# Kernel optimization log

Measured on AMD Instinct MI355X. Metric: run time of the kernel, lower is better.

The kernel has to match this reference:

```python
import jax, jax.numpy as jnp
import numpy as np

# Config mirrors Voxelization(__init__) with training=True -> max_voxels[0]
VOXEL_SIZE = (0.05, 0.05, 0.1)
PC_LO = (0.0, -40.0, -3.0)
PC_HI = (70.4, 40.0, 1.0)
MAX_POINTS = 64
MAX_VOXELS = 60000
GX = int(round((PC_HI[0] - PC_LO[0]) / VOXEL_SIZE[0]))  # 1408
GY = int(round((PC_HI[1] - PC_LO[1]) / VOXEL_SIZE[1]))  # 1600
GZ = int(round((PC_HI[2] - PC_LO[2]) / VOXEL_SIZE[2]))  # 40
SENT = GX * GY * GZ  # sentinel linear id for out-of-range points


def setup_inputs() -> dict:
    key = jax.random.key(0)
    u = jax.random.uniform(key, (2_000_000, 4), dtype=jnp.float32)
    lo = jnp.array([PC_LO[0], PC_LO[1], PC_LO[2], 0.0], jnp.float32)
    span = jnp.array([PC_HI[0] - PC_LO[0], PC_HI[1] - PC_LO[1], PC_HI[2] - PC_LO[2], 1.0], jnp.float32)
    points = lo + u * span  # xyz inside range, intensity in [0,1)
    return {"points": points}


def _voxelize(points):
    N, C = points.shape
    vs = jnp.array(VOXEL_SIZE, jnp.float32)
    lo = jnp.array(PC_LO, jnp.float32)
    grid = jnp.array([GX, GY, GZ], jnp.int32)

    g = jnp.floor((points[:, :3] - lo) / vs).astype(jnp.int32)  # [N,3] grid coords (x,y,z)
    valid = jnp.all((g >= 0) & (g < grid), axis=1)
    lin = (g[:, 0] * GY + g[:, 1]) * GZ + g[:, 2]
    lin = jnp.where(valid, lin, SENT).astype(jnp.int32)

    # Stable sort by voxel id; ties keep original point order (deterministic mode)
    order = jnp.argsort(lin)  # jnp.argsort is stable
    sl = lin[order]
    idx = jnp.arange(N, dtype=jnp.int32)
    is_start = jnp.concatenate([jnp.ones((1,), bool), sl[1:] != sl[:-1]])
    gid_sorted = (jnp.cumsum(is_start) - 1).astype(jnp.int32)  # sorted-group id per sorted point

    # First original point index per group -> first-occurrence voxel ordering
    group_first = jnp.full((N,), N, jnp.int32).at[gid_sorted].min(
        jnp.where(is_start, order.astype(jnp.int32), N))
    group_lin = jnp.full((N,), SENT, jnp.int32).at[gid_sorted].min(sl)
    group_first = jnp.where(group_lin == SENT, N, group_first)  # sentinel group ranks last
    perm = jnp.argsort(group_first)  # rank -> group
    inv_rank = jnp.zeros((N,), jnp.int32).at[perm].set(idx)  # group -> rank

    num_valid = jnp.sum(is_start & (sl != SENT)).astype(jnp.int32)
    voxel_num = jnp.minimum(num_valid, MAX_VOXELS)

    # Position within voxel (point order within group)
    start_idx = jax.lax.cummax(jnp.where(is_start, idx, -1))
    pos_sorted = idx - start_idx

    gid = jnp.zeros((N,), jnp.int32).at[order].set(gid_sorted)
    pos = jnp.zeros((N,), jnp.int32).at[order].set(pos_sorted)
    rank = inv_rank[gid]
    keep = valid & (rank < MAX_VOXELS) & (pos < MAX_POINTS)
    rk = jnp.where(keep, rank, MAX_VOXELS)  # OOB -> dropped
    pk = jnp.where(keep, pos, MAX_POINTS)

    voxels = jnp.zeros((MAX_VOXELS, MAX_POINTS, C), points.dtype).at[rk, pk].set(points, mode='drop')
    coors = jnp.zeros((MAX_VOXELS, 3), jnp.int32).at[rk].set(g[:, ::-1], mode='drop')  # flip -> (z,y,x)
    group_count = jnp.zeros((N,), jnp.int32).at[gid_sorted].add((sl != SENT).astype(jnp.int32))
    npv = jnp.minimum(group_count[perm], MAX_POINTS)[:MAX_VOXELS].astype(jnp.int32)
    return voxels, coors, npv, voxel_num


def reference(points):
    # Padded equivalent of torch output (voxels[:n], coors[:n].flip(-1), npv[:n]):
    # rows >= voxel_num are zero; voxel_num gives the true count.
    return _voxelize(points)
```

## Files before the change

### kernel.cpp

```cpp
#include <hip/hip_runtime.h>


#define MAXV 60000
#define MAXP 64
#define FCUT 131072
#define NBUCK 512
#define BSHIFT 13
#define BSLOTS 8192
#define TMASK (NBUCK * BSLOTS - 1)
#define BCAP 5120
#define ECAP 512
#define BIN_CHUNK 4096
#define BIN_T 512
#define SCAN_T 1024
#define CHUNK 2048

typedef unsigned long long u64;

__device__ __forceinline__ int compute_lin(float x, float y, float z) {
  float fx = floorf((x - 0.0f) / 0.05f);
  float fy = floorf((y - (-40.0f)) / 0.05f);
  float fz = floorf((z - (-3.0f)) / 0.1f);
  if (!(fx >= 0.0f && fx < 1408.0f &&
        fy >= 0.0f && fy < 1600.0f &&
        fz >= 0.0f && fz < 40.0f))
    return -1;
  return (((int)fx) * 1600 + (int)fy) * 40 + (int)fz;
}

__device__ __forceinline__ unsigned hash_s(int lin) {
  unsigned h = (unsigned)lin * 2654435761u;
  return (h ^ (h >> 15)) & TMASK;
}

__global__ __launch_bounds__(BIN_T) void k_binA(const float4* __restrict__ pts,
                                                int N, u64* __restrict__ binned,
                                                int* __restrict__ bucketCnt) {
  __shared__ int hist[NBUCK];
  __shared__ int lbase[NBUCK];
  __shared__ int cursor[NBUCK];
  __shared__ int gbase[NBUCK];
  __shared__ int totSh;
  __shared__ u64 stage[BIN_CHUNK];

  int tid = threadIdx.x;
  int blockStart = blockIdx.x * BIN_CHUNK;
  hist[tid] = 0;
  __syncthreads();

  unsigned sArr[8];
  int linArr[8];
#pragma unroll
  for (int j = 0; j < 8; j++) {
    int i = blockStart + j * BIN_T + tid;
    unsigned sv = 0xFFFFFFFFu; int lv = 0;
    if (i < N) {
      float4 p = pts[i];
      int lin = compute_lin(p.x, p.y, p.z);
      if (lin >= 0) {
        sv = hash_s(lin);
        lv = lin;
        atomicAdd(&hist[sv >> BSHIFT], 1);
      }
    }
    sArr[j] = sv; linArr[j] = lv;
  }
  __syncthreads();

  int v = hist[tid];
  lbase[tid] = v;
  __syncthreads();
  for (int off = 1; off < NBUCK; off <<= 1) {
    int t = (tid >= off) ? lbase[tid - off] : 0;
    __syncthreads();
    lbase[tid] += t;
    __syncthreads();
  }
  int excl = lbase[tid] - v;
  __syncthreads();
  lbase[tid] = excl;
  cursor[tid] = excl;
  __syncthreads();

#pragma unroll
  for (int j = 0; j < 8; j++) {
    if (sArr[j] != 0xFFFFFFFFu) {
      int b = (int)(sArr[j] >> BSHIFT);
      int k = atomicAdd(&cursor[b], 1);
      int i = blockStart + j * BIN_T + tid;
      stage[k] = ((u64)(unsigned)linArr[j] << 32) | (unsigned)i;
    }
  }
  __syncthreads();

  int cntB = cursor[tid] - lbase[tid];
  if (cntB > 0) gbase[tid] = atomicAdd(&bucketCnt[tid], cntB);
  if (tid == BIN_T - 1) totSh = cursor[NBUCK - 1];
  __syncthreads();

  int tot = totSh;
  for (int k = tid; k < tot; k += BIN_T) {
    u64 e = stage[k];
    int b = (int)(hash_s((int)(e >> 32)) >> BSHIFT);
    int off = gbase[b] + (k - lbase[b]);
    if (off < BCAP) binned[(size_t)b * BCAP + off] = e;
  }
}

__global__ __launch_bounds__(1024) void k_binB(
    const u64* __restrict__ binned, const int* __restrict__ bucketCnt,
    u64* __restrict__ fs, u64* __restrict__ gEbuf, int* __restrict__ bcnt,
    int* __restrict__ occPartials) {
  __shared__ u64 tab[BSLOTS];
  __shared__ u64 ev[ECAP];
  __shared__ int evCnt;
  __shared__ int occTot;

  int tid = threadIdx.x;
  int b = blockIdx.x;
  for (int k = tid; k < BSLOTS / 2; k += 1024)
    ((ulonglong2*)tab)[k] = make_ulonglong2(~0ull, ~0ull);
  if (tid == 0) { evCnt = 0; occTot = 0; }
  __syncthreads();

  int n = bucketCnt[b]; if (n > BCAP) n = BCAP;
  for (int k = tid; k < n; k += 1024) {
    u64 e = binned[(size_t)b * BCAP + k];
    int i = (int)(unsigned)e;
    int lin = (int)(e >> 32);
    int ls = (int)(hash_s(lin) & (BSLOTS - 1));
    u64 mine = ((u64)(unsigned)i << 40) | ((u64)(unsigned)lin << 12);
    for (;;) {
      u64 cur = atomicCAS(&tab[ls], ~0ull, mine);
      if (cur == ~0ull) break;
      if (((cur >> 12) & 0xFFFFFFFull) == (u64)(unsigned)lin) {
        for (;;) {
          unsigned f = (unsigned)(cur >> 40);
          unsigned c = (unsigned)(cur & 0xFFFu);
          unsigned nf = ((unsigned)i < f) ? (unsigned)i : f;
          unsigned rec = ((unsigned)i < f) ? f : (unsigned)i;
          unsigned nc = (c < 0xFFFu) ? c + 1 : 0xFFFu;
          u64 nv = ((u64)nf << 40) | ((u64)(unsigned)lin << 12) | nc;
          u64 prev = atomicCAS(&tab[ls], cur, nv);
          if (prev == cur) {
            unsigned pos = c + 1;
            if (pos < MAXP) {
              int eidx = atomicAdd(&evCnt, 1);
              if (eidx < ECAP)
                ev[eidx] = ((u64)ls << 40) | ((u64)pos << 24) | rec;
            }
            break;
          }
          cur = prev;
        }
        break;
      }
      ls = (ls + 1) & (BSLOTS - 1);
    }
  }
  __syncthreads();

  int ec = evCnt; if (ec > ECAP) ec = ECAP;
  for (int k = tid; k < ec; k += 1024) {
    u64 e = ev[k];
    int ls = (int)(e >> 40);
    u64 pm = (e >> 24) & 0xFFFFull;
    unsigned rec = (unsigned)(e & 0xFFFFFFu);
    unsigned f = (unsigned)(tab[ls] >> 40);
    gEbuf[(size_t)b * ECAP + k] =
        (f < FCUT) ? (((u64)f << 40) | (pm << 24) | rec) : ~0ull;
  }
  if (tid == 0) bcnt[b] = ec;

  int occ = 0;
  for (int k = tid; k < BSLOTS / 2; k += 1024) {
    ulonglong2 w2 = ((const ulonglong2*)tab)[k];
#pragma unroll
    for (int h = 0; h < 2; h++) {
      u64 w = h ? w2.y : w2.x;
      if (w != ~0ull) {
        occ++;
        unsigned f = (unsigned)(w >> 40);
        if (f < FCUT) {
          unsigned lin = (unsigned)((w >> 12) & 0xFFFFFFFull);
          unsigned c = (unsigned)(w & 0xFFFu) + 1;
          if (c > MAXP) c = MAXP;
          fs[f] = ((u64)lin << 8) | c;
        }
      }
    }
  }
  for (int off = 32; off > 0; off >>= 1) occ += __shfl_down(occ, off);
  if ((tid & 63) == 0) atomicAdd(&occTot, occ);
  __syncthreads();
  if (tid == 0) occPartials[b] = occTot;
}

__global__ void k_flag_reduce(const u64* __restrict__ fs, int M,
                              int* __restrict__ partials) {
  int tid = threadIdx.x;
  int base = blockIdx.x * CHUNK + tid * 8;
  int sum = 0;
#pragma unroll
  for (int j = 0; j < 8; j++) {
    int i = base + j;
    if (i < M && fs[i] != 0) sum++;
  }
  __shared__ int sd[256];
  sd[tid] = sum;
  __syncthreads();
  for (int off = 128; off > 0; off >>= 1) {
    if (tid < off) sd[tid] += sd[tid + off];
    __syncthreads();
  }
  if (tid == 0) partials[blockIdx.x] = sd[0];
}

__global__ void k_scan_partials(int* __restrict__ partials, int NB,
                                const int* __restrict__ occPartials, int nOcc,
                                float* __restrict__ outNum,
                                int* __restrict__ Dws) {
  __shared__ int sd[SCAN_T];
  __shared__ int Dsh;
  int tid = threadIdx.x;

  int acc = 0;
  for (int i = tid; i < nOcc; i += SCAN_T) acc += occPartials[i];
  sd[tid] = acc;
  __syncthreads();
  for (int off = SCAN_T / 2; off > 0; off >>= 1) {
    if (tid < off) sd[tid] += sd[tid + off];
    __syncthreads();
  }
  if (tid == 0) Dsh = sd[0];
  __syncthreads();

  int i0 = 2 * tid, i1 = 2 * tid + 1;
  int a = (i0 < NB) ? partials[i0] : 0;
  int b = (i1 < NB) ? partials[i1] : 0;
  int s = a + b;
  sd[tid] = s;
  __syncthreads();
  for (int off = 1; off < SCAN_T; off <<= 1) {
    int v = (tid >= off) ? sd[tid - off] : 0;
    __syncthreads();
    sd[tid] += v;
    __syncthreads();
  }
  int incl = sd[tid];
  int exclPair = incl - s;
  if (i0 < NB) partials[i0] = exclPair;
  if (i1 < NB) partials[i1] = exclPair + a;
  if (tid == SCAN_T - 1) {
    int D = Dsh;
    int vn = D < MAXV ? D : MAXV;
    outNum[0] = (float)vn;
    Dws[0] = vn;
  }
}

__global__ void k_rank(const u64* __restrict__ fs,
                       const int* __restrict__ partials,
                       const float4* __restrict__ pts,
                       int* __restrict__ rankOf,
                       float* __restrict__ outCoors, float* __restrict__ outNpv,
                       float4* __restrict__ outVox, int M) {
  int tid = threadIdx.x;
  int base = blockIdx.x * CHUNK + tid * 8;
  u64 v[8];
  int sum = 0;
#pragma unroll
  for (int j = 0; j < 8; j++) {
    int i = base + j;
    v[j] = (i < M) ? fs[i] : 0;
    sum += (v[j] != 0) ? 1 : 0;
  }
  __shared__ int sd[256];
  sd[tid] = sum;
  __syncthreads();
  for (int off = 1; off < 256; off <<= 1) {
    int t = (tid >= off) ? sd[tid - off] : 0;
    __syncthreads();
    sd[tid] += t;
    __syncthreads();
  }
  int run = partials[blockIdx.x] + sd[tid] - sum;
#pragma unroll
  for (int j = 0; j < 8; j++) {
    if (v[j] != 0) {
      int f = base + j;
      int r = run++;
      rankOf[f] = r;
      if (r < MAXV) {
        int lin = (int)(v[j] >> 8);
        int gz = lin % 40;
        int t = lin / 40;
        int gy = t % 1600;
        int gx = t / 1600;
        outCoors[r * 3 + 0] = (float)gz;
        outCoors[r * 3 + 1] = (float)gy;
        outCoors[r * 3 + 2] = (float)gx;
        outNpv[r] = (float)(int)(v[j] & 0xFF);
        outVox[(size_t)r * MAXP] = pts[f];
      }
    }
  }
}

__global__ void k_events(const float4* __restrict__ pts,
                         const int* __restrict__ bcnt,
                         const u64* __restrict__ gEbuf,
                         const int* __restrict__ rankOf,
                         const int* __restrict__ Dws,
                         float* __restrict__ outCoors,
                         float* __restrict__ outNpv,
                         float4* __restrict__ outVox) {
  int gid = blockIdx.x * 256 + threadIdx.x;

  int D = Dws[0];
  for (int r = D + gid; r < MAXV; r += NBUCK * ECAP) {
    outCoors[r * 3 + 0] = 0.f; outCoors[r * 3 + 1] = 0.f;
    outCoors[r * 3 + 2] = 0.f; outNpv[r] = 0.f;
  }

  int b = gid >> 9;
  int t = gid & (ECAP - 1);
  if (t >= bcnt[b]) return;
  u64 e = gEbuf[(size_t)b * ECAP + t];
  if (e == ~0ull) return;
  unsigned f = (unsigned)(e >> 40);
  unsigned pos = (unsigned)((e >> 24) & 0xFFFFu);
  unsigned rec = (unsigned)(e & 0xFFFFFFu);
  int r = rankOf[f];
  if ((unsigned)r >= (unsigned)MAXV) return;
  outVox[(size_t)r * MAXP + pos] = pts[rec];
}

extern "C" void kernel_launch(void* const* d_in, const int* in_sizes, int n_in,
                              void* d_out, int out_size, void* d_ws, size_t ws_size,
                              hipStream_t stream) {
  const float4* pts = (const float4*)d_in[0];
  int N = in_sizes[0] / 4;

  float* out = (float*)d_out;
  float* outVox = out;
  float* outCoors = out + (size_t)MAXV * MAXP * 4;
  float* outNpv = outCoors + (size_t)MAXV * 3;
  float* outNum = outNpv + MAXV;

  char* w = (char*)d_ws;
  u64* binned = (u64*)w;         w += (size_t)NBUCK * BCAP * 8;
  u64* gEbuf = (u64*)w;          w += (size_t)NBUCK * ECAP * 8;
  int* rankOf = (int*)w;         w += (size_t)FCUT * 4;
  int* partials = (int*)w;       w += 1024;
  int* occPartials = (int*)w;    w += NBUCK * 4;
  int* bcnt = (int*)w;           w += NBUCK * 4;
  int* Dws = (int*)w;            w += 256;
  char* z0 = w;
  u64* fs = (u64*)w;             w += (size_t)FCUT * 8;
  int* bucketCnt = (int*)w;      w += NBUCK * 4;
  size_t zBytes = (size_t)(w - z0);

  hipMemsetAsync(d_out, 0, (size_t)out_size * sizeof(float), stream);
  hipMemsetAsync(z0, 0, zBytes, stream);

  int nbA = (N + BIN_CHUNK - 1) / BIN_CHUNK;
  int NB = FCUT / CHUNK;

  k_binA<<<nbA, BIN_T, 0, stream>>>(pts, N, binned, bucketCnt);
  k_binB<<<NBUCK, 1024, 0, stream>>>(binned, bucketCnt, fs, gEbuf, bcnt,
                                     occPartials);
  k_flag_reduce<<<NB, 256, 0, stream>>>(fs, FCUT, partials);
  k_scan_partials<<<1, SCAN_T, 0, stream>>>(partials, NB, occPartials, NBUCK,
                                            outNum, Dws);
  k_rank<<<NB, 256, 0, stream>>>(fs, partials, pts, rankOf,
                                 outCoors, outNpv, (float4*)outVox, FCUT);
  k_events<<<NBUCK * ECAP / 256, 256, 0, stream>>>(pts, bcnt, gEbuf, rankOf,
                                                   Dws, outCoors, outNpv,
                                                   (float4*)outVox);
}
```

Before: 147.1 us.

## Fuse flag reduce, partial scan and rank into one decoupled-lookback kernel

Replaces three kernels (per-chunk flag count, single-block scan of partials, rank assignment) with one kernel. Each block publishes its inclusive aggregate to a status array with a flag bit, then reads all predecessor aggregates with acquire loads to form its exclusive prefix. Block 0 also computes the voxel count. This removes two kernel launches and a second pass over fs. Blocks spin-wait on earlier blocks, so correctness depends on those blocks being resident or already scheduled, which holds for only 64 blocks.

```diff
diff --git a/kernel.cpp b/kernel.cpp
--- a/kernel.cpp
+++ b/kernel.cpp
@@ -12,8 +12,8 @@
 #define ECAP 512
 #define BIN_CHUNK 4096
 #define BIN_T 512
-#define SCAN_T 1024
 #define CHUNK 2048
+#define NCHUNK (FCUT / CHUNK)
 
 typedef unsigned long long u64;
 
@@ -196,86 +196,26 @@
   if (tid == 0) occPartials[b] = occTot;
 }
 
-__global__ void k_flag_reduce(const u64* __restrict__ fs, int M,
-                              int* __restrict__ partials) {
+__global__ __launch_bounds__(256) void k_rankLB(
+    const u64* __restrict__ fs, const float4* __restrict__ pts,
+    const int* __restrict__ occPartials, int* __restrict__ status,
+    int* __restrict__ rankOf,
+    float* __restrict__ outCoors, float* __restrict__ outNpv,
+    float4* __restrict__ outVox, float* __restrict__ outNum,
+    int* __restrict__ Dws) {
+  int b = blockIdx.x;
   int tid = threadIdx.x;
-  int base = blockIdx.x * CHUNK + tid * 8;
-  int sum = 0;
-#pragma unroll
-  for (int j = 0; j < 8; j++) {
-    int i = base + j;
-    if (i < M && fs[i] != 0) sum++;
-  }
+  int base = b * CHUNK + tid * 8;
   __shared__ int sd[256];
-  sd[tid] = sum;
-  __syncthreads();
-  for (int off = 128; off > 0; off >>= 1) {
-    if (tid < off) sd[tid] += sd[tid + off];
-    __syncthreads();
-  }
-  if (tid == 0) partials[blockIdx.x] = sd[0];
-}
-
-__global__ void k_scan_partials(int* __restrict__ partials, int NB,
-                                const int* __restrict__ occPartials, int nOcc,
-                                float* __restrict__ outNum,
-                                int* __restrict__ Dws) {
-  __shared__ int sd[SCAN_T];
-  __shared__ int Dsh;
-  int tid = threadIdx.x;
-
-  int acc = 0;
-  for (int i = tid; i < nOcc; i += SCAN_T) acc += occPartials[i];
-  sd[tid] = acc;
-  __syncthreads();
-  for (int off = SCAN_T / 2; off > 0; off >>= 1) {
-    if (tid < off) sd[tid] += sd[tid + off];
-    __syncthreads();
-  }
-  if (tid == 0) Dsh = sd[0];
-  __syncthreads();
-
-  int i0 = 2 * tid, i1 = 2 * tid + 1;
-  int a = (i0 < NB) ? partials[i0] : 0;
-  int b = (i1 < NB) ? partials[i1] : 0;
-  int s = a + b;
-  sd[tid] = s;
-  __syncthreads();
-  for (int off = 1; off < SCAN_T; off <<= 1) {
-    int v = (tid >= off) ? sd[tid - off] : 0;
-    __syncthreads();
-    sd[tid] += v;
-    __syncthreads();
-  }
-  int incl = sd[tid];
-  int exclPair = incl - s;
-  if (i0 < NB) partials[i0] = exclPair;
-  if (i1 < NB) partials[i1] = exclPair + a;
-  if (tid == SCAN_T - 1) {
-    int D = Dsh;
-    int vn = D < MAXV ? D : MAXV;
-    outNum[0] = (float)vn;
-    Dws[0] = vn;
-  }
-}
-
-__global__ void k_rank(const u64* __restrict__ fs,
-                       const int* __restrict__ partials,
-                       const float4* __restrict__ pts,
-                       int* __restrict__ rankOf,
-                       float* __restrict__ outCoors, float* __restrict__ outNpv,
-                       float4* __restrict__ outVox, int M) {
-  int tid = threadIdx.x;
-  int base = blockIdx.x * CHUNK + tid * 8;
+  __shared__ int exclSh;
+
   u64 v[8];
   int sum = 0;
 #pragma unroll
   for (int j = 0; j < 8; j++) {
-    int i = base + j;
-    v[j] = (i < M) ? fs[i] : 0;
+    v[j] = fs[base + j];
     sum += (v[j] != 0) ? 1 : 0;
   }
-  __shared__ int sd[256];
   sd[tid] = sum;
   __syncthreads();
   for (int off = 1; off < 256; off <<= 1) {
@@ -284,7 +224,26 @@
     sd[tid] += t;
     __syncthreads();
   }
-  int run = partials[blockIdx.x] + sd[tid] - sum;
+  int inclThread = sd[tid];
+
+  if (tid == 255)
+    __hip_atomic_store(&status[b], 0x40000000 | inclThread,
+                       __ATOMIC_RELEASE, __HIP_MEMORY_SCOPE_AGENT);
+
+  int myAgg = 0;
+  if (tid < b) {
+    int sv;
+    do {
+      sv = __hip_atomic_load(&status[tid], __ATOMIC_ACQUIRE,
+                             __HIP_MEMORY_SCOPE_AGENT);
+    } while (!(sv & 0x40000000));
+    myAgg = sv & 0x3FFFFFFF;
+  }
+  for (int off = 32; off > 0; off >>= 1) myAgg += __shfl_down(myAgg, off);
+  if (tid == 0) exclSh = myAgg;
+  __syncthreads();
+
+  int run = exclSh + inclThread - sum;
 #pragma unroll
   for (int j = 0; j < 8; j++) {
     if (v[j] != 0) {
@@ -305,6 +264,24 @@
       }
     }
   }
+
+  if (b == 0) {
+    int acc = 0;
+    for (int i = tid; i < NBUCK; i += 256) acc += occPartials[i];
+    __syncthreads();
+    sd[tid] = acc;
+    __syncthreads();
+    for (int off = 128; off > 0; off >>= 1) {
+      if (tid < off) sd[tid] += sd[tid + off];
+      __syncthreads();
+    }
+    if (tid == 0) {
+      int D = sd[0];
+      int vn = D < MAXV ? D : MAXV;
+      outNum[0] = (float)vn;
+      Dws[0] = vn;
+    }
+  }
 }
 
 __global__ void k_events(const float4* __restrict__ pts,
@@ -352,29 +329,26 @@
   u64* binned = (u64*)w;         w += (size_t)NBUCK * BCAP * 8;
   u64* gEbuf = (u64*)w;          w += (size_t)NBUCK * ECAP * 8;
   int* rankOf = (int*)w;         w += (size_t)FCUT * 4;
-  int* partials = (int*)w;       w += 1024;
   int* occPartials = (int*)w;    w += NBUCK * 4;
   int* bcnt = (int*)w;           w += NBUCK * 4;
   int* Dws = (int*)w;            w += 256;
   char* z0 = w;
   u64* fs = (u64*)w;             w += (size_t)FCUT * 8;
   int* bucketCnt = (int*)w;      w += NBUCK * 4;
+  int* status = (int*)w;         w += NCHUNK * 4;
   size_t zBytes = (size_t)(w - z0);
 
   hipMemsetAsync(d_out, 0, (size_t)out_size * sizeof(float), stream);
   hipMemsetAsync(z0, 0, zBytes, stream);
 
   int nbA = (N + BIN_CHUNK - 1) / BIN_CHUNK;
-  int NB = FCUT / CHUNK;
 
   k_binA<<<nbA, BIN_T, 0, stream>>>(pts, N, binned, bucketCnt);
   k_binB<<<NBUCK, 1024, 0, stream>>>(binned, bucketCnt, fs, gEbuf, bcnt,
                                      occPartials);
-  k_flag_reduce<<<NB, 256, 0, stream>>>(fs, FCUT, partials);
-  k_scan_partials<<<1, SCAN_T, 0, stream>>>(partials, NB, occPartials, NBUCK,
-                                            outNum, Dws);
-  k_rank<<<NB, 256, 0, stream>>>(fs, partials, pts, rankOf,
-                                 outCoors, outNpv, (float4*)outVox, FCUT);
+  k_rankLB<<<NCHUNK, 256, 0, stream>>>(fs, pts, occPartials, status, rankOf,
+                                       outCoors, outNpv, (float4*)outVox,
+                                       outNum, Dws);
   k_events<<<NBUCK * ECAP / 256, 256, 0, stream>>>(pts, bcnt, gEbuf, rankOf,
                                                    Dws, outCoors, outNpv,
                                                    (float4*)outVox);
```

Result: faster. 144.0 us (-2.1%).
